# Kernel optimization log

Hardware: AMD Instinct MI355X
Metric: run time of the kernel (lower is better)

## Reference

```python
import jax, jax.numpy as jnp
import numpy as np


def setup_inputs() -> dict:
    key = jax.random.key(0)
    ks = jax.random.split(key, 6)
    S, B, I, H = 1024, 128, 256, 256
    scale = 1.0 / np.sqrt(H)
    return {
        "x": jax.random.normal(ks[0], (S, B, I), dtype=jnp.float32),
        "h0": jax.random.normal(ks[1], (B, H), dtype=jnp.float32),
        "weight_ih": jax.random.normal(ks[2], (3 * H, I), dtype=jnp.float32) * scale,
        "weight_hh_t": jax.random.normal(ks[3], (H, 3 * H), dtype=jnp.float32) * scale,
        "bias_ih": jax.random.normal(ks[4], (3 * H,), dtype=jnp.float32) * scale,
        "bias_hh": jax.random.normal(ks[5], (3 * H,), dtype=jnp.float32) * scale,
    }


def reference(x, h0, weight_ih, weight_hh_t, bias_ih, bias_hh):
    # x: [S, B, I]; h0: [B, H]
    H = h0.shape[-1]
    # Precompute input-side gate projections for all timesteps: [S, B, 3H]
    x_gates = jnp.einsum("sbi,gi->sbg", x, weight_ih) + bias_ih

    def step(h_prev, xg):  # h_prev: [B, H], xg: [B, 3H]
        gh = h_prev @ weight_hh_t + bias_hh  # [B, 3H]
        r = jax.nn.sigmoid(xg[:, :H] + gh[:, :H])
        z = jax.nn.sigmoid(xg[:, H:2 * H] + gh[:, H:2 * H])
        n = jnp.tanh(xg[:, 2 * H:] + r * gh[:, 2 * H:])
        h_next = (1.0 - z) * n + z * h_prev
        return h_next, h_next

    h_final, h_out = jax.lax.scan(step, h0, x_gates)
    return h_out, h_final
```

## Files before the change

kernel.cpp:

```cpp
#include <hip/hip_runtime.h>
#include <hip/hip_bf16.h>

typedef __attribute__((ext_vector_type(8))) short bf16x8;
typedef __attribute__((ext_vector_type(4))) float f32x4;
typedef __attribute__((ext_vector_type(4))) unsigned short u16x4;

static __device__ __forceinline__ unsigned short f2bf(float f) {
  unsigned u = __builtin_bit_cast(unsigned, f);
  u += 0x7FFFu + ((u >> 16) & 1u);
  return (unsigned short)(u >> 16);
}
static __device__ __forceinline__ float bf2f(unsigned short h) {
  unsigned u = ((unsigned)h) << 16;
  return __builtin_bit_cast(float, u);
}
static __device__ __forceinline__ float sigm(float x) {
  return __builtin_amdgcn_rcpf(1.0f + __builtin_amdgcn_exp2f(x * -1.44269504088896f));
}
static __device__ __forceinline__ float tanh_fast(float x) {
  float e = __builtin_amdgcn_exp2f(x * 2.88539008177793f);
  return 1.0f - 2.0f * __builtin_amdgcn_rcpf(1.0f + e);
}

__global__ __launch_bounds__(256) void gru_xgates(
    const float* __restrict__ x,
    const float* __restrict__ w_ih,
    const float* __restrict__ b_ih,
    const float* __restrict__ b_hh,
    unsigned short* __restrict__ xg)
{
  __shared__ unsigned short Al[128][40];
  __shared__ unsigned short Bl[128][40];

  const int t = threadIdx.x;
  const int lane = t & 63;
  const int w = t >> 6;
  const int l15 = lane & 15;
  const int lhi = lane >> 4;
  const int m0 = blockIdx.y * 128;
  const int g0 = blockIdx.x * 128;
  const int wm = (w >> 1) * 64;
  const int wn = (w & 1) * 64;
  const int r_st = t >> 3;
  const int k_st = (t & 7) * 4;

  f32x4 acc[4][4];
  #pragma unroll
  for (int mt = 0; mt < 4; ++mt)
    #pragma unroll
    for (int nt = 0; nt < 4; ++nt) acc[mt][nt] = (f32x4){0.f, 0.f, 0.f, 0.f};

  float bias[4];
  #pragma unroll
  for (int nt = 0; nt < 4; ++nt) {
    const int col = g0 + wn + nt * 16 + l15;
    bias[nt] = b_ih[col] + (col < 512 ? b_hh[col] : 0.f);
  }

  for (int kt = 0; kt < 8; ++kt) {
    const int k0 = kt * 32 + k_st;
    #pragma unroll
    for (int q = 0; q < 4; ++q) {
      const int r = r_st + q * 32;
      float4 a = *(const float4*)(x + (size_t)(m0 + r) * 256 + k0);
      float4 b = *(const float4*)(w_ih + (size_t)(g0 + r) * 256 + k0);
      *(u16x4*)&Al[r][k_st] = (u16x4){f2bf(a.x), f2bf(a.y), f2bf(a.z), f2bf(a.w)};
      *(u16x4*)&Bl[r][k_st] = (u16x4){f2bf(b.x), f2bf(b.y), f2bf(b.z), f2bf(b.w)};
    }
    __syncthreads();

    bf16x8 af[4], bfv[4];
    #pragma unroll
    for (int i = 0; i < 4; ++i) {
      af[i]  = *(const bf16x8*)&Al[wm + i * 16 + l15][lhi * 8];
      bfv[i] = *(const bf16x8*)&Bl[wn + i * 16 + l15][lhi * 8];
    }
    #pragma unroll
    for (int mt = 0; mt < 4; ++mt)
      #pragma unroll
      for (int nt = 0; nt < 4; ++nt)
        acc[mt][nt] = __builtin_amdgcn_mfma_f32_16x16x32_bf16(af[mt], bfv[nt], acc[mt][nt], 0, 0, 0);
    __syncthreads();
  }

  #pragma unroll
  for (int mt = 0; mt < 4; ++mt)
    #pragma unroll
    for (int nt = 0; nt < 4; ++nt)
      #pragma unroll
      for (int q = 0; q < 4; ++q) {
        const int row = m0 + wm + mt * 16 + lhi * 4 + q;
        const int col = g0 + wn + nt * 16 + l15;
        xg[(size_t)row * 768 + col] = f2bf(acc[mt][nt][q] + bias[nt]);
      }
}

__global__ __launch_bounds__(512) void gru_rec(
    const float* __restrict__ hin,
    const float* __restrict__ w_hh,
    const float* __restrict__ b_hh,
    const unsigned short* __restrict__ xg,
    float* __restrict__ hstate,
    float* __restrict__ out,
    int s0, int steps)
{
  __shared__ unsigned short hb[2][4096];

  const int t = threadIdx.x;
  const int lane = t & 63;
  const int w = t >> 6;
  const int l15 = lane & 15;
  const int lhi = lane >> 4;
  const int B0 = blockIdx.x * 16;
  const int swz = (l15 & 7) << 4;
  const int cbase = w * 32 + lhi * 4;

  bf16x8 wf[8][6];
  #pragma unroll
  for (int nt = 0; nt < 6; ++nt) {
    const int col = (nt >> 1) * 256 + w * 32 + (nt & 1) * 16 + l15;
    #pragma unroll
    for (int kt = 0; kt < 8; ++kt) {
      bf16x8 v;
      #pragma unroll
      for (int e = 0; e < 8; ++e)
        v[e] = (short)f2bf(w_hh[(size_t)(kt * 32 + lhi * 8 + e) * 768 + col]);
      wf[kt][nt] = v;
    }
  }

  u16x4 biasn[2];
  #pragma unroll
  for (int half = 0; half < 2; ++half) {
    f32x4 bv = *(const f32x4*)(b_hh + 512 + cbase + half * 16);
    biasn[half] = (u16x4){f2bf(bv[0]), f2bf(bv[1]), f2bf(bv[2]), f2bf(bv[3])};
  }

  f32x4 hp[2];
  #pragma unroll
  for (int half = 0; half < 2; ++half) {
    hp[half] = *(const f32x4*)(hin + (size_t)(B0 + l15) * 256 + cbase + half * 16);
    const int off = l15 * 512 + (((cbase + half * 16) * 2) ^ swz);
    *(u16x4*)((char*)hb[0] + off) =
        (u16x4){f2bf(hp[half][0]), f2bf(hp[half][1]), f2bf(hp[half][2]), f2bf(hp[half][3])};
  }

  const unsigned short* xp = xg + (size_t)(B0 + l15) * 768 + cbase;
  u16x4 xgv[6];
  #pragma unroll
  for (int g = 0; g < 3; ++g)
    #pragma unroll
    for (int half = 0; half < 2; ++half)
      xgv[g * 2 + half] = *(const u16x4*)(xp + g * 256 + half * 16);

  float* op = out + (size_t)(B0 + l15) * 256 + cbase;
  __syncthreads();

  #pragma unroll 1
  for (int s = 0; s < steps; ++s) {
    const char* hcur = (const char*)hb[s & 1];
    char* hnxt = (char*)hb[(s & 1) ^ 1];

    f32x4 acc[6];
    acc[0] = acc[1] = acc[2] = acc[3] = (f32x4){0.f, 0.f, 0.f, 0.f};
    acc[4] = (f32x4){bf2f(biasn[0][0]), bf2f(biasn[0][1]), bf2f(biasn[0][2]), bf2f(biasn[0][3])};
    acc[5] = (f32x4){bf2f(biasn[1][0]), bf2f(biasn[1][1]), bf2f(biasn[1][2]), bf2f(biasn[1][3])};

    #pragma unroll
    for (int kt = 0; kt < 8; ++kt) {
      bf16x8 hf = *(const bf16x8*)(hcur + l15 * 512 + ((kt * 64 + lhi * 16) ^ swz));
      #pragma unroll
      for (int nt = 0; nt < 6; ++nt)
        acc[nt] = __builtin_amdgcn_mfma_f32_16x16x32_bf16(wf[kt][nt], hf, acc[nt], 0, 0, 0);
    }

    #pragma unroll
    for (int half = 0; half < 2; ++half) {
      f32x4 hn;
      #pragma unroll
      for (int q = 0; q < 4; ++q) {
        const float r = sigm(bf2f(xgv[half][q]) + acc[half][q]);
        const float z = sigm(bf2f(xgv[2 + half][q]) + acc[2 + half][q]);
        const float n = tanh_fast(bf2f(xgv[4 + half][q]) + r * acc[4 + half][q]);
        hn[q] = n + z * (hp[half][q] - n);
      }
      hp[half] = hn;
      const int off = l15 * 512 + (((cbase + half * 16) * 2) ^ swz);
      *(u16x4*)(hnxt + off) =
          (u16x4){f2bf(hn[0]), f2bf(hn[1]), f2bf(hn[2]), f2bf(hn[3])};
      *(f32x4*)(op + (size_t)(s0 + s) * 32768 + half * 16) = hn;
    }

    xp += (s + 1 < steps) ? 98304 : 0;
    #pragma unroll
    for (int g = 0; g < 3; ++g)
      #pragma unroll
      for (int half = 0; half < 2; ++half)
        xgv[g * 2 + half] = *(const u16x4*)(xp + g * 256 + half * 16);

    __syncthreads();
  }

  #pragma unroll
  for (int half = 0; half < 2; ++half) {
    *(f32x4*)(hstate + (size_t)(B0 + l15) * 256 + cbase + half * 16) = hp[half];
    *(f32x4*)(op + (size_t)1024 * 32768 + half * 16) = hp[half];
  }
}

extern "C" void kernel_launch(void* const* d_in, const int* in_sizes, int n_in,
                              void* d_out, int out_size, void* d_ws, size_t ws_size,
                              hipStream_t stream) {
  const float* x    = (const float*)d_in[0];
  const float* h0   = (const float*)d_in[1];
  const float* w_ih = (const float*)d_in[2];
  const float* w_hh = (const float*)d_in[3];
  const float* b_ih = (const float*)d_in[4];
  const float* b_hh = (const float*)d_in[5];
  float* out = (float*)d_out;

  float* hstate = (float*)d_ws;
  unsigned short* xg = (unsigned short*)((char*)d_ws + 131072);
  const size_t avail = ws_size > 131072 ? ws_size - 131072 : 0;

  int C = 1024;
  while (C > 1 && (size_t)C * 196608ull > avail) C >>= 1;

  for (int c0 = 0; c0 < 1024; c0 += C) {
    gru_xgates<<<dim3(6, C), 256, 0, stream>>>(x + (size_t)c0 * 32768, w_ih, b_ih, b_hh, xg);
    gru_rec<<<dim3(8), 512, 0, stream>>>(c0 == 0 ? h0 : hstate, w_hh, b_hh, xg,
                                         hstate, out, c0, C);
  }
}
```

Measured before the change: 4.220 ms.

## Widen xgates tile to 256 columns and move GRU hidden state into LDS

The input-projection GEMM now uses 128x256 tiles. Each block covers more gate columns, so the x tile is converted and loaded fewer times, and loads are restructured per thread. In the recurrent kernel, the fp32 previous hidden state and the n-gate bias move from registers to LDS, and both kernels get a min-blocks-per-CU launch bound, aiming to relieve register pressure from the 48 held weight fragments. Next-step xgate loads are also issued earlier, interleaved with the gate math, to hide latency on the serial recurrence. Costs include extra LDS traffic per step and more accumulator registers in the GEMM.

```diff
diff --git a/kernel.cpp b/kernel.cpp
--- a/kernel.cpp
+++ b/kernel.cpp
@@ -22,7 +22,7 @@
   return 1.0f - 2.0f * __builtin_amdgcn_rcpf(1.0f + e);
 }
 
-__global__ __launch_bounds__(256) void gru_xgates(
+__global__ __launch_bounds__(256, 2) void gru_xgates(
     const float* __restrict__ x,
     const float* __restrict__ w_ih,
     const float* __restrict__ b_ih,
@@ -30,7 +30,7 @@
     unsigned short* __restrict__ xg)
 {
   __shared__ unsigned short Al[128][40];
-  __shared__ unsigned short Bl[128][40];
+  __shared__ unsigned short Bl[256][40];
 
   const int t = threadIdx.x;
   const int lane = t & 63;
@@ -38,47 +38,52 @@
   const int l15 = lane & 15;
   const int lhi = lane >> 4;
   const int m0 = blockIdx.y * 128;
-  const int g0 = blockIdx.x * 128;
+  const int g0 = blockIdx.x * 256;
   const int wm = (w >> 1) * 64;
-  const int wn = (w & 1) * 64;
-  const int r_st = t >> 3;
-  const int k_st = (t & 7) * 4;
-
-  f32x4 acc[4][4];
+  const int wn = (w & 1) * 128;
+  const int rA = t >> 1;
+  const int kq = (t & 1) * 16;
+
+  f32x4 acc[4][8];
   #pragma unroll
   for (int mt = 0; mt < 4; ++mt)
     #pragma unroll
-    for (int nt = 0; nt < 4; ++nt) acc[mt][nt] = (f32x4){0.f, 0.f, 0.f, 0.f};
-
-  float bias[4];
-  #pragma unroll
-  for (int nt = 0; nt < 4; ++nt) {
+    for (int nt = 0; nt < 8; ++nt) acc[mt][nt] = (f32x4){0.f, 0.f, 0.f, 0.f};
+
+  float bias[8];
+  #pragma unroll
+  for (int nt = 0; nt < 8; ++nt) {
     const int col = g0 + wn + nt * 16 + l15;
     bias[nt] = b_ih[col] + (col < 512 ? b_hh[col] : 0.f);
   }
 
   for (int kt = 0; kt < 8; ++kt) {
-    const int k0 = kt * 32 + k_st;
-    #pragma unroll
-    for (int q = 0; q < 4; ++q) {
-      const int r = r_st + q * 32;
-      float4 a = *(const float4*)(x + (size_t)(m0 + r) * 256 + k0);
-      float4 b = *(const float4*)(w_ih + (size_t)(g0 + r) * 256 + k0);
-      *(u16x4*)&Al[r][k_st] = (u16x4){f2bf(a.x), f2bf(a.y), f2bf(a.z), f2bf(a.w)};
-      *(u16x4*)&Bl[r][k_st] = (u16x4){f2bf(b.x), f2bf(b.y), f2bf(b.z), f2bf(b.w)};
+    const int k0 = kt * 32 + kq;
+    #pragma unroll
+    for (int i = 0; i < 4; ++i) {
+      float4 a = *(const float4*)(x + (size_t)(m0 + rA) * 256 + k0 + i * 4);
+      *(u16x4*)&Al[rA][kq + i * 4] = (u16x4){f2bf(a.x), f2bf(a.y), f2bf(a.z), f2bf(a.w)};
+    }
+    #pragma unroll
+    for (int h2 = 0; h2 < 2; ++h2) {
+      const int rB = rA + h2 * 128;
+      #pragma unroll
+      for (int i = 0; i < 4; ++i) {
+        float4 b = *(const float4*)(w_ih + (size_t)(g0 + rB) * 256 + k0 + i * 4);
+        *(u16x4*)&Bl[rB][kq + i * 4] = (u16x4){f2bf(b.x), f2bf(b.y), f2bf(b.z), f2bf(b.w)};
+      }
     }
     __syncthreads();
 
-    bf16x8 af[4], bfv[4];
-    #pragma unroll
-    for (int i = 0; i < 4; ++i) {
-      af[i]  = *(const bf16x8*)&Al[wm + i * 16 + l15][lhi * 8];
-      bfv[i] = *(const bf16x8*)&Bl[wn + i * 16 + l15][lhi * 8];
-    }
+    bf16x8 af[4], bfv[8];
+    #pragma unroll
+    for (int i = 0; i < 4; ++i) af[i] = *(const bf16x8*)&Al[wm + i * 16 + l15][lhi * 8];
+    #pragma unroll
+    for (int nt = 0; nt < 8; ++nt) bfv[nt] = *(const bf16x8*)&Bl[wn + nt * 16 + l15][lhi * 8];
     #pragma unroll
     for (int mt = 0; mt < 4; ++mt)
       #pragma unroll
-      for (int nt = 0; nt < 4; ++nt)
+      for (int nt = 0; nt < 8; ++nt)
         acc[mt][nt] = __builtin_amdgcn_mfma_f32_16x16x32_bf16(af[mt], bfv[nt], acc[mt][nt], 0, 0, 0);
     __syncthreads();
   }
@@ -86,7 +91,7 @@
   #pragma unroll
   for (int mt = 0; mt < 4; ++mt)
     #pragma unroll
-    for (int nt = 0; nt < 4; ++nt)
+    for (int nt = 0; nt < 8; ++nt)
       #pragma unroll
       for (int q = 0; q < 4; ++q) {
         const int row = m0 + wm + mt * 16 + lhi * 4 + q;
@@ -95,7 +100,7 @@
       }
 }
 
-__global__ __launch_bounds__(512) void gru_rec(
+__global__ __launch_bounds__(512, 2) void gru_rec(
     const float* __restrict__ hin,
     const float* __restrict__ w_hh,
     const float* __restrict__ b_hh,
@@ -105,6 +110,8 @@
     int s0, int steps)
 {
   __shared__ unsigned short hb[2][4096];
+  __shared__ float hpf[16][256];
+  __shared__ float bias_lds[256];
 
   const int t = threadIdx.x;
   const int lane = t & 63;
@@ -129,20 +136,15 @@
     }
   }
 
-  u16x4 biasn[2];
+  if (t < 256) bias_lds[t] = b_hh[512 + t];
+
   #pragma unroll
   for (int half = 0; half < 2; ++half) {
-    f32x4 bv = *(const f32x4*)(b_hh + 512 + cbase + half * 16);
-    biasn[half] = (u16x4){f2bf(bv[0]), f2bf(bv[1]), f2bf(bv[2]), f2bf(bv[3])};
-  }
-
-  f32x4 hp[2];
-  #pragma unroll
-  for (int half = 0; half < 2; ++half) {
-    hp[half] = *(const f32x4*)(hin + (size_t)(B0 + l15) * 256 + cbase + half * 16);
-    const int off = l15 * 512 + (((cbase + half * 16) * 2) ^ swz);
-    *(u16x4*)((char*)hb[0] + off) =
-        (u16x4){f2bf(hp[half][0]), f2bf(hp[half][1]), f2bf(hp[half][2]), f2bf(hp[half][3])};
+    const int c = cbase + half * 16;
+    f32x4 h = *(const f32x4*)(hin + (size_t)(B0 + l15) * 256 + c);
+    *(f32x4*)((char*)hpf + l15 * 1024 + ((c * 4) ^ swz)) = h;
+    *(u16x4*)((char*)hb[0] + l15 * 512 + ((c * 2) ^ swz)) =
+        (u16x4){f2bf(h[0]), f2bf(h[1]), f2bf(h[2]), f2bf(h[3])};
   }
 
   const unsigned short* xp = xg + (size_t)(B0 + l15) * 768 + cbase;
@@ -153,7 +155,7 @@
     for (int half = 0; half < 2; ++half)
       xgv[g * 2 + half] = *(const u16x4*)(xp + g * 256 + half * 16);
 
-  float* op = out + (size_t)(B0 + l15) * 256 + cbase;
+  float* op = out + (size_t)s0 * 32768 + (size_t)(B0 + l15) * 256 + cbase;
   __syncthreads();
 
   #pragma unroll 1
@@ -163,8 +165,8 @@
 
     f32x4 acc[6];
     acc[0] = acc[1] = acc[2] = acc[3] = (f32x4){0.f, 0.f, 0.f, 0.f};
-    acc[4] = (f32x4){bf2f(biasn[0][0]), bf2f(biasn[0][1]), bf2f(biasn[0][2]), bf2f(biasn[0][3])};
-    acc[5] = (f32x4){bf2f(biasn[1][0]), bf2f(biasn[1][1]), bf2f(biasn[1][2]), bf2f(biasn[1][3])};
+    acc[4] = *(const f32x4*)&bias_lds[cbase];
+    acc[5] = *(const f32x4*)&bias_lds[cbase + 16];
 
     #pragma unroll
     for (int kt = 0; kt < 8; ++kt) {
@@ -174,37 +176,41 @@
         acc[nt] = __builtin_amdgcn_mfma_f32_16x16x32_bf16(wf[kt][nt], hf, acc[nt], 0, 0, 0);
     }
 
+    const unsigned short* xpn = xp + (s + 1 < steps ? 98304 : 0);
+
     #pragma unroll
     for (int half = 0; half < 2; ++half) {
+      const int c = cbase + half * 16;
+      f32x4 hp = *(const f32x4*)((const char*)hpf + l15 * 1024 + ((c * 4) ^ swz));
       f32x4 hn;
       #pragma unroll
       for (int q = 0; q < 4; ++q) {
         const float r = sigm(bf2f(xgv[half][q]) + acc[half][q]);
         const float z = sigm(bf2f(xgv[2 + half][q]) + acc[2 + half][q]);
         const float n = tanh_fast(bf2f(xgv[4 + half][q]) + r * acc[4 + half][q]);
-        hn[q] = n + z * (hp[half][q] - n);
+        hn[q] = n + z * (hp[q] - n);
       }
-      hp[half] = hn;
-      const int off = l15 * 512 + (((cbase + half * 16) * 2) ^ swz);
-      *(u16x4*)(hnxt + off) =
+      xgv[half]     = *(const u16x4*)(xpn + half * 16);
+      xgv[2 + half] = *(const u16x4*)(xpn + 256 + half * 16);
+      xgv[4 + half] = *(const u16x4*)(xpn + 512 + half * 16);
+
+      *(f32x4*)((char*)hpf + l15 * 1024 + ((c * 4) ^ swz)) = hn;
+      *(u16x4*)(hnxt + l15 * 512 + ((c * 2) ^ swz)) =
           (u16x4){f2bf(hn[0]), f2bf(hn[1]), f2bf(hn[2]), f2bf(hn[3])};
-      *(f32x4*)(op + (size_t)(s0 + s) * 32768 + half * 16) = hn;
-    }
-
-    xp += (s + 1 < steps) ? 98304 : 0;
-    #pragma unroll
-    for (int g = 0; g < 3; ++g)
-      #pragma unroll
-      for (int half = 0; half < 2; ++half)
-        xgv[g * 2 + half] = *(const u16x4*)(xp + g * 256 + half * 16);
-
+      *(f32x4*)(op + half * 16) = hn;
+    }
+
+    xp = xpn;
+    op += 32768;
     __syncthreads();
   }
 
   #pragma unroll
   for (int half = 0; half < 2; ++half) {
-    *(f32x4*)(hstate + (size_t)(B0 + l15) * 256 + cbase + half * 16) = hp[half];
-    *(f32x4*)(op + (size_t)1024 * 32768 + half * 16) = hp[half];
+    const int c = cbase + half * 16;
+    f32x4 h = *(const f32x4*)((const char*)hpf + l15 * 1024 + ((c * 4) ^ swz));
+    *(f32x4*)(hstate + (size_t)(B0 + l15) * 256 + c) = h;
+    *(f32x4*)(out + (size_t)1024 * 32768 + (size_t)(B0 + l15) * 256 + c) = h;
   }
 }
 
@@ -227,7 +233,7 @@
   while (C > 1 && (size_t)C * 196608ull > avail) C >>= 1;
 
   for (int c0 = 0; c0 < 1024; c0 += C) {
-    gru_xgates<<<dim3(6, C), 256, 0, stream>>>(x + (size_t)c0 * 32768, w_ih, b_ih, b_hh, xg);
+    gru_xgates<<<dim3(3, C), 256, 0, stream>>>(x + (size_t)c0 * 32768, w_ih, b_ih, b_hh, xg);
     gru_rec<<<dim3(8), 512, 0, stream>>>(c0 == 0 ? h0 : hstate, w_hh, b_hh, xg,
                                          hstate, out, c0, C);
   }
```

Measured after the change: 3.650 ms. 13.5% less time.
